# Performance work log

Hardware: AMD Instinct MI355X
Metric: run time of the kernel (lower is better)

The kernel has to match this reference:

```python
import jax, jax.numpy as jnp
import numpy as np

N_NODES = 50000
N_EDGES = 800000
HIDDEN = 128


def setup_inputs() -> dict:
    key = jax.random.key(0)
    k1, k2, k3, k4, k5, k6 = jax.random.split(key, 6)
    node_features = jax.random.normal(k1, (N_NODES, HIDDEN), dtype=jnp.float32)
    senders = jax.random.randint(k2, (N_EDGES,), 0, N_NODES, dtype=jnp.int32)
    receivers = jax.random.randint(k3, (N_EDGES,), 0, N_NODES, dtype=jnp.int32)
    edge_features = jax.random.normal(k4, (N_EDGES, HIDDEN), dtype=jnp.float32)
    # message_proj: Linear(3H, H); torch default init ~ U(-1/sqrt(fan_in), 1/sqrt(fan_in))
    bound = 1.0 / np.sqrt(3 * HIDDEN)
    W = jax.random.uniform(k5, (3 * HIDDEN, HIDDEN), dtype=jnp.float32, minval=-bound, maxval=bound)
    b = jax.random.uniform(k6, (HIDDEN,), dtype=jnp.float32, minval=-bound, maxval=bound)
    ln_w = jnp.ones((HIDDEN,), dtype=jnp.float32)
    ln_b = jnp.zeros((HIDDEN,), dtype=jnp.float32)
    return {"node_features": node_features, "senders": senders, "receivers": receivers,
            "edge_features": edge_features, "W": W, "b": b, "ln_w": ln_w, "ln_b": ln_b}


def layer_norm(x, w, b, eps=1e-5):
    mu = jnp.mean(x, axis=-1, keepdims=True)
    var = jnp.mean(jnp.square(x - mu), axis=-1, keepdims=True)
    return (x - mu) * jax.lax.rsqrt(var + eps) * w + b


def reference(node_features, senders, receivers, edge_features, W, b, ln_w, ln_b):
    # gather endpoints, concat along feature dim: [E, 3H]
    cat = jnp.concatenate((node_features[senders], node_features[receivers], edge_features), axis=-1)
    message = jax.nn.relu(cat @ W + b)  # [E, H]
    # scatter-add messages back to receiver nodes ('sum' aggregation)
    aggr = jax.ops.segment_sum(message, receivers, num_segments=node_features.shape[0])
    out = node_features + aggr  # residual
    return layer_norm(out, ln_w, ln_b)
```

## Files before the change

kernel.cpp:

```cpp
#include <hip/hip_runtime.h>

#define H 128
#define NSRC 3
#define MSTRIDE 132

typedef _Float16 f16;
typedef _Float16 f16x2 __attribute__((ext_vector_type(2)));
typedef _Float16 f16x4 __attribute__((ext_vector_type(4)));
typedef _Float16 f16x8 __attribute__((ext_vector_type(8)));
typedef float f32x4 __attribute__((ext_vector_type(4)));

__global__ void setup_kernel(const float* __restrict__ W, f16* __restrict__ wbuf,
                             int* __restrict__ cnt, float4* __restrict__ AGG4,
                             int n_nodes, int nagg4,
                             const float* __restrict__ nf, f16* __restrict__ nfh,
                             int nf4) {
    const int i = blockIdx.x * blockDim.x + threadIdx.x;
    const int np = gridDim.x * blockDim.x;
    if (i < NSRC * H * H) {
        int src = i >> 14;
        int k = (i >> 7) & 127;
        int c = i & 127;
        float v = W[((size_t)src * H + k) * H + c];
        unsigned off = ((unsigned)(c * 256 + k * 2)) ^ ((unsigned)((c & 7) << 4));
        wbuf[(size_t)src * (H * H) + (off >> 1)] = (f16)v;
    }
    if (i < n_nodes) cnt[i] = 0;
    for (int j = i; j < nagg4; j += np) AGG4[j] = make_float4(0.f, 0.f, 0.f, 0.f);
    for (int j = i; j < nf4; j += np) {
        float4 v = ((const float4*)nf)[j];
        f16x4 h;
        h[0] = (f16)v.x; h[1] = (f16)v.y; h[2] = (f16)v.z; h[3] = (f16)v.w;
        ((f16x4*)nfh)[j] = h;
    }
}

__global__ void hist_kernel(const int* __restrict__ recv, int* __restrict__ cnt, int n_edges) {
    int e = (blockIdx.x * blockDim.x + threadIdx.x) * 4;
    if (e + 3 < n_edges) {
        int4 r = *(const int4*)&recv[e];
        atomicAdd(&cnt[r.x], 1);
        atomicAdd(&cnt[r.y], 1);
        atomicAdd(&cnt[r.z], 1);
        atomicAdd(&cnt[r.w], 1);
    } else {
        for (int j = e; j < n_edges; ++j) atomicAdd(&cnt[recv[j]], 1);
    }
}

__global__ void scan_kernel(const int* __restrict__ cnt, int* __restrict__ row_ptr,
                            int* __restrict__ cursor, int n) {
    __shared__ int sd[1024];
    const int t = threadIdx.x;
    const int per = (n + 1023) >> 10;
    const int st = t * per;
    const int en = min(st + per, n);
    int s = 0;
    for (int i = st; i < en; ++i) s += cnt[i];
    sd[t] = s;
    __syncthreads();
    for (int off = 1; off < 1024; off <<= 1) {
        int v = 0;
        if (t >= off) v = sd[t - off];
        __syncthreads();
        sd[t] += v;
        __syncthreads();
    }
    int run = sd[t] - s;
    for (int i = st; i < en; ++i) {
        row_ptr[i] = run;
        cursor[i] = run;
        run += cnt[i];
    }
    if (t == 1023) row_ptr[n] = sd[1023];
}

__global__ void scatter_kernel(const int* __restrict__ send, const int* __restrict__ recv,
                               int* __restrict__ cursor, int* __restrict__ perm,
                               int2* __restrict__ ssr, int n_edges) {
    int e = blockIdx.x * blockDim.x + threadIdx.x;
    if (e < n_edges) {
        int r = recv[e];
        int pos = atomicAdd(&cursor[r], 1);
        perm[pos] = e;
        ssr[pos] = make_int2(send[e], r);
    }
}

__global__ __launch_bounds__(256, 2)
void fused_msg_kernel(const f16* __restrict__ nfh, const float* __restrict__ ef,
                      const int* __restrict__ perm, const int2* __restrict__ ssr,
                      const f16* __restrict__ wbuf, const float* __restrict__ b,
                      float* __restrict__ AGG, int n_edges) {
    __shared__ __align__(16) f16 Alds[NSRC * 64 * H];
    __shared__ __align__(16) f16 MSG[64 * MSTRIDE];
    __shared__ int SR[64];

    const int t = threadIdx.x;
    const int lane = t & 63;
    const int wid = t >> 6;
    const int l15 = lane & 15;
    const int lg = lane >> 4;
    const int c2 = lane * 2;

    f16x8 breg[NSRC][2][4];
#pragma unroll
    for (int src = 0; src < NSRC; ++src)
#pragma unroll
        for (int cf = 0; cf < 2; ++cf)
#pragma unroll
            for (int ks = 0; ks < 4; ++ks) {
                const int c = wid * 32 + cf * 16 + l15;
                const int k = ks * 32 + lg * 8;
                unsigned off = ((unsigned)(c * 256 + k * 2)) ^ ((unsigned)((c & 7) << 4));
                breg[src][cf][ks] =
                    *(const f16x8*)((const char*)wbuf + (size_t)src * 32768 + off);
            }

    const float2 bias2 = *(const float2*)&b[c2];
    const int srow = t >> 2;
    const int sq = t & 3;
    const int ntiles = (n_edges + 63) >> 6;
    const int stride = gridDim.x;

    int cr = 0;
    int ns = 0, nr = 0, npx = 0;
    int4 s0, s1, s2, s3;
    int4 r0, r1, r2, r3;
    float4 e0, e1, e2, e3, e4, e5, e6, e7;

    int tile = blockIdx.x;
    if (tile < ntiles) {
        const int e = min(tile * 64 + srow, n_edges - 1);
        int2 cv = ssr[e];
        int cs = cv.x; cr = cv.y;
        int cp = perm[e];
        const int4* ps = (const int4*)(nfh + (size_t)cs * H + sq * 32);
        s0 = ps[0]; s1 = ps[1]; s2 = ps[2]; s3 = ps[3];
        const int4* pr = (const int4*)(nfh + (size_t)cr * H + sq * 32);
        r0 = pr[0]; r1 = pr[1]; r2 = pr[2]; r3 = pr[3];
        const float4* pe = (const float4*)(ef + (size_t)cp * H + sq * 32);
        e0 = pe[0]; e1 = pe[1]; e2 = pe[2]; e3 = pe[3];
        e4 = pe[4]; e5 = pe[5]; e6 = pe[6]; e7 = pe[7];
    }
    if (tile + stride < ntiles) {
        const int e = min((tile + stride) * 64 + srow, n_edges - 1);
        int2 nv = ssr[e];
        ns = nv.x; nr = nv.y;
        npx = perm[e];
    }

    for (; tile < ntiles; tile += stride) {
        const int e0base = tile * 64;
        __syncthreads();

        {
            unsigned off0 = ((unsigned)(srow * 256 + (sq * 32 + 0) * 2)) ^ ((unsigned)((srow & 7) << 4));
            unsigned off1 = ((unsigned)(srow * 256 + (sq * 32 + 8) * 2)) ^ ((unsigned)((srow & 7) << 4));
            unsigned off2 = ((unsigned)(srow * 256 + (sq * 32 + 16) * 2)) ^ ((unsigned)((srow & 7) << 4));
            unsigned off3 = ((unsigned)(srow * 256 + (sq * 32 + 24) * 2)) ^ ((unsigned)((srow & 7) << 4));
            *(int4*)((char*)Alds + off0) = s0;
            *(int4*)((char*)Alds + off1) = s1;
            *(int4*)((char*)Alds + off2) = s2;
            *(int4*)((char*)Alds + off3) = s3;
            *(int4*)((char*)Alds + 16384 + off0) = r0;
            *(int4*)((char*)Alds + 16384 + off1) = r1;
            *(int4*)((char*)Alds + 16384 + off2) = r2;
            *(int4*)((char*)Alds + 16384 + off3) = r3;
            f16x8 h0, h1, h2, h3;
#pragma unroll
            for (int j = 0; j < 4; ++j) { h0[j] = (f16)(&e0.x)[j]; h0[j + 4] = (f16)(&e1.x)[j]; }
#pragma unroll
            for (int j = 0; j < 4; ++j) { h1[j] = (f16)(&e2.x)[j]; h1[j + 4] = (f16)(&e3.x)[j]; }
#pragma unroll
            for (int j = 0; j < 4; ++j) { h2[j] = (f16)(&e4.x)[j]; h2[j + 4] = (f16)(&e5.x)[j]; }
#pragma unroll
            for (int j = 0; j < 4; ++j) { h3[j] = (f16)(&e6.x)[j]; h3[j + 4] = (f16)(&e7.x)[j]; }
            *(f16x8*)((char*)Alds + 32768 + off0) = h0;
            *(f16x8*)((char*)Alds + 32768 + off1) = h1;
            *(f16x8*)((char*)Alds + 32768 + off2) = h2;
            *(f16x8*)((char*)Alds + 32768 + off3) = h3;
            if (sq == 0) SR[srow] = cr;
        }

        int t2s = 0, t2r = 0, t2p = 0;
        if (tile + 2 * stride < ntiles) {
            const int e = min((tile + 2 * stride) * 64 + srow, n_edges - 1);
            int2 t2v = ssr[e];
            t2s = t2v.x; t2r = t2v.y;
            t2p = perm[e];
        }
        if (tile + stride < ntiles) {
            const int4* ps = (const int4*)(nfh + (size_t)ns * H + sq * 32);
            s0 = ps[0]; s1 = ps[1]; s2 = ps[2]; s3 = ps[3];
            const int4* pr = (const int4*)(nfh + (size_t)nr * H + sq * 32);
            r0 = pr[0]; r1 = pr[1]; r2 = pr[2]; r3 = pr[3];
            const float4* pe = (const float4*)(ef + (size_t)npx * H + sq * 32);
            e0 = pe[0]; e1 = pe[1]; e2 = pe[2]; e3 = pe[3];
            e4 = pe[4]; e5 = pe[5]; e6 = pe[6]; e7 = pe[7];
        }
        __syncthreads();

        f32x4 acc[4][2];
#pragma unroll
        for (int rf = 0; rf < 4; ++rf) {
            acc[rf][0] = (f32x4){0.f, 0.f, 0.f, 0.f};
            acc[rf][1] = (f32x4){0.f, 0.f, 0.f, 0.f};
        }
#pragma unroll
        for (int src = 0; src < NSRC; ++src)
#pragma unroll
            for (int ks = 0; ks < 4; ++ks) {
                f16x8 af[4];
#pragma unroll
                for (int rf = 0; rf < 4; ++rf) {
                    const int row = rf * 16 + l15;
                    const int k = ks * 32 + lg * 8;
                    unsigned off = ((unsigned)(row * 256 + k * 2))
                                   ^ ((unsigned)((row & 7) << 4));
                    af[rf] = *(const f16x8*)((const char*)Alds + (size_t)src * 16384 + off);
                }
#pragma unroll
                for (int rf = 0; rf < 4; ++rf) {
                    acc[rf][0] = __builtin_amdgcn_mfma_f32_16x16x32_f16(
                        af[rf], breg[src][0][ks], acc[rf][0], 0, 0, 0);
                    acc[rf][1] = __builtin_amdgcn_mfma_f32_16x16x32_f16(
                        af[rf], breg[src][1][ks], acc[rf][1], 0, 0, 0);
                }
            }

#pragma unroll
        for (int rf = 0; rf < 4; ++rf)
#pragma unroll
            for (int cf = 0; cf < 2; ++cf)
#pragma unroll
                for (int q = 0; q < 4; ++q)
                    MSG[(rf * 16 + lg * 4 + q) * MSTRIDE + wid * 32 + cf * 16 + l15] =
                        (f16)acc[rf][cf][q];
        __syncthreads();

        int rarr[16];
#pragma unroll
        for (int j = 0; j < 16; ++j) rarr[j] = SR[wid * 16 + j];
        float ax = 0.f, ay = 0.f;
#pragma unroll
        for (int j = 0; j < 16; ++j) {
            const int e = e0base + wid * 16 + j;
            if (e < n_edges) {
                f16x2 m = *(const f16x2*)&MSG[(wid * 16 + j) * MSTRIDE + c2];
                ax += fmaxf((float)m[0] + bias2.x, 0.f);
                ay += fmaxf((float)m[1] + bias2.y, 0.f);
                bool flush = (j == 15) || (e + 1 >= n_edges) || (rarr[j + 1] != rarr[j]);
                if (flush) {
                    atomicAdd(&AGG[(size_t)rarr[j] * H + c2], ax);
                    atomicAdd(&AGG[(size_t)rarr[j] * H + c2 + 1], ay);
                    ax = 0.f;
                    ay = 0.f;
                }
            }
        }

        cr = nr;
        ns = t2s; nr = t2r; npx = t2p;
    }
}

__global__ __launch_bounds__(256, 4)
void ln_agg_kernel(const float* __restrict__ nf, const float* __restrict__ AGG,
                   const float* __restrict__ lnw, const float* __restrict__ lnb,
                   float* __restrict__ out, int n_nodes) {
    const int wv = threadIdx.x >> 6;
    const int lane = threadIdx.x & 63;
    const int row = blockIdx.x * (blockDim.x >> 6) + wv;
    if (row >= n_nodes) return;
    float2 a = ((const float2*)(nf + (size_t)row * H))[lane];
    float2 g = ((const float2*)(AGG + (size_t)row * H))[lane];
    float vx = a.x + g.x, vy = a.y + g.y;

    float s = vx + vy;
#pragma unroll
    for (int m = 32; m; m >>= 1) s += __shfl_xor(s, m, 64);
    float mu = s * (1.f / H);
    float dx = vx - mu, dy = vy - mu;
    float q = dx * dx + dy * dy;
#pragma unroll
    for (int m = 32; m; m >>= 1) q += __shfl_xor(q, m, 64);
    float rs = rsqrtf(q * (1.f / H) + 1e-5f);

    float2 w2 = ((const float2*)lnw)[lane];
    float2 b2 = ((const float2*)lnb)[lane];
    float2 o;
    o.x = dx * rs * w2.x + b2.x;
    o.y = dy * rs * w2.y + b2.y;
    ((float2*)(out + (size_t)row * H))[lane] = o;
}

__global__ void naive_edge_kernel(const float* __restrict__ nf, const int* __restrict__ s,
                                  const int* __restrict__ r, const float* __restrict__ ef,
                                  const float* __restrict__ W, const float* __restrict__ b,
                                  float* __restrict__ out, int n_edges) {
    int e = blockIdx.x * 2 + (threadIdx.x >> 7);
    int c = threadIdx.x & 127;
    if (e >= n_edges) return;
    int se = s[e], re = r[e];
    float acc = b[c];
    for (int k = 0; k < H; ++k) {
        acc += nf[(size_t)se * H + k] * W[(size_t)k * H + c];
        acc += nf[(size_t)re * H + k] * W[(size_t)(H + k) * H + c];
        acc += ef[(size_t)e * H + k] * W[(size_t)(2 * H + k) * H + c];
    }
    atomicAdd(&out[(size_t)re * H + c], fmaxf(acc, 0.f));
}

__global__ __launch_bounds__(256, 4)
void ln_kernel(const float* __restrict__ nf, const float* __restrict__ lnw,
               const float* __restrict__ lnb, float* __restrict__ out, int n_nodes) {
    const int wv = threadIdx.x >> 6;
    const int lane = threadIdx.x & 63;
    const int row = blockIdx.x * (blockDim.x >> 6) + wv;
    if (row >= n_nodes) return;
    float2 a = ((const float2*)(nf + (size_t)row * H))[lane];
    float2 g = ((float2*)(out + (size_t)row * H))[lane];
    float vx = a.x + g.x, vy = a.y + g.y;
    float s = vx + vy;
#pragma unroll
    for (int m = 32; m; m >>= 1) s += __shfl_xor(s, m, 64);
    float mu = s * (1.f / H);
    float dx = vx - mu, dy = vy - mu;
    float q = dx * dx + dy * dy;
#pragma unroll
    for (int m = 32; m; m >>= 1) q += __shfl_xor(q, m, 64);
    float rs = rsqrtf(q * (1.f / H) + 1e-5f);
    float2 w2 = ((const float2*)lnw)[lane];
    float2 b2 = ((const float2*)lnb)[lane];
    float2 o;
    o.x = dx * rs * w2.x + b2.x;
    o.y = dy * rs * w2.y + b2.y;
    ((float2*)(out + (size_t)row * H))[lane] = o;
}

extern "C" void kernel_launch(void* const* d_in, const int* in_sizes, int n_in,
                              void* d_out, int out_size, void* d_ws, size_t ws_size,
                              hipStream_t stream) {
    const float* nf        = (const float*)d_in[0];
    const int*   senders   = (const int*)d_in[1];
    const int*   receivers = (const int*)d_in[2];
    const float* ef        = (const float*)d_in[3];
    const float* W         = (const float*)d_in[4];
    const float* b         = (const float*)d_in[5];
    const float* lnw       = (const float*)d_in[6];
    const float* lnb       = (const float*)d_in[7];
    float* out = (float*)d_out;

    const int n_nodes = in_sizes[0] / H;
    const int n_edges = in_sizes[1];
    const int nfelem = n_nodes * H;

    size_t o = 0;
    auto carve = [&](size_t bytes) { size_t r = o; o += (bytes + 255) & ~(size_t)255; return r; };
    const size_t o_wbuf   = carve((size_t)NSRC * H * H * sizeof(f16));
    const size_t o_nfh    = carve((size_t)nfelem * sizeof(f16));
    const size_t o_cnt    = carve((size_t)n_nodes * 4);
    const size_t o_rowptr = carve((size_t)(n_nodes + 1) * 4);
    const size_t o_cursor = carve((size_t)n_nodes * 4);
    const size_t o_perm   = carve((size_t)n_edges * 4);
    const size_t o_ssr    = carve((size_t)n_edges * 8);
    const size_t o_agg    = carve((size_t)nfelem * sizeof(float));
    const size_t need_full = o;

    char* ws = (char*)d_ws;

    if (ws_size >= need_full) {
        f16* wbuf   = (f16*)(ws + o_wbuf);
        f16* nfh    = (f16*)(ws + o_nfh);
        int* cnt    = (int*)(ws + o_cnt);
        int* rowptr = (int*)(ws + o_rowptr);
        int* cursor = (int*)(ws + o_cursor);
        int* perm   = (int*)(ws + o_perm);
        int2* ssr   = (int2*)(ws + o_ssr);
        float* AGG  = (float*)(ws + o_agg);

        setup_kernel<<<2048, 256, 0, stream>>>(W, wbuf, cnt, (float4*)AGG,
                                               n_nodes, nfelem / 4, nf, nfh, nfelem / 4);
        hist_kernel<<<(n_edges / 4 + 255) / 256, 256, 0, stream>>>(receivers, cnt, n_edges);
        scan_kernel<<<1, 1024, 0, stream>>>(cnt, rowptr, cursor, n_nodes);
        scatter_kernel<<<(n_edges + 255) / 256, 256, 0, stream>>>(
            senders, receivers, cursor, perm, ssr, n_edges);

        fused_msg_kernel<<<1024, 256, 0, stream>>>(nfh, ef, perm, ssr, wbuf, b,
                                                   AGG, n_edges);
        ln_agg_kernel<<<(n_nodes + 3) / 4, 256, 0, stream>>>(nf, AGG, lnw, lnb, out, n_nodes);
    } else {
        hipMemsetAsync(d_out, 0, (size_t)nfelem * sizeof(float), stream);
        naive_edge_kernel<<<(n_edges + 1) / 2, 256, 0, stream>>>(
            nf, senders, receivers, ef, W, b, out, n_edges);
        ln_kernel<<<(n_nodes + 3) / 4, 256, 0, stream>>>(nf, lnw, lnb, out, n_nodes);
    }
}
```

Baseline: 384.3 us.

## Load edge features directly into MFMA fragments, shrink LDS, raise occupancy

Edge-feature rows are no longer staged through LDS. Each wave now loads its fp32 edge rows straight from global memory into MFMA A-fragments, converts them to f16 in registers, and issues the third-source MFMAs from those. This cuts LDS by a third and removes the prefetched receiver and edge registers, so launch bounds go to 3 blocks per CU and the grid to 1536. In exchange, the receiver and edge loads are no longer prefetched a tile ahead, so their global latency is exposed inside the loop. Each edge row is also fetched by all four waves, which adds redundant global traffic that only the cache can absorb.

```diff
diff --git a/kernel.cpp b/kernel.cpp
--- a/kernel.cpp
+++ b/kernel.cpp
@@ -87,12 +87,12 @@
     }
 }
 
-__global__ __launch_bounds__(256, 2)
+__global__ __launch_bounds__(256, 3)
 void fused_msg_kernel(const f16* __restrict__ nfh, const float* __restrict__ ef,
                       const int* __restrict__ perm, const int2* __restrict__ ssr,
                       const f16* __restrict__ wbuf, const float* __restrict__ b,
                       float* __restrict__ AGG, int n_edges) {
-    __shared__ __align__(16) f16 Alds[NSRC * 64 * H];
+    __shared__ __align__(16) f16 Alds[2 * 64 * H];
     __shared__ __align__(16) f16 MSG[64 * MSTRIDE];
     __shared__ int SR[64];
 
@@ -124,35 +124,32 @@
     const int stride = gridDim.x;
 
     int cr = 0;
-    int ns = 0, nr = 0, npx = 0;
+    int ns = 0, nr = 0;
+    int t2s = 0, t2r = 0;
     int4 s0, s1, s2, s3;
-    int4 r0, r1, r2, r3;
-    float4 e0, e1, e2, e3, e4, e5, e6, e7;
 
     int tile = blockIdx.x;
     if (tile < ntiles) {
         const int e = min(tile * 64 + srow, n_edges - 1);
         int2 cv = ssr[e];
         int cs = cv.x; cr = cv.y;
-        int cp = perm[e];
         const int4* ps = (const int4*)(nfh + (size_t)cs * H + sq * 32);
         s0 = ps[0]; s1 = ps[1]; s2 = ps[2]; s3 = ps[3];
-        const int4* pr = (const int4*)(nfh + (size_t)cr * H + sq * 32);
-        r0 = pr[0]; r1 = pr[1]; r2 = pr[2]; r3 = pr[3];
-        const float4* pe = (const float4*)(ef + (size_t)cp * H + sq * 32);
-        e0 = pe[0]; e1 = pe[1]; e2 = pe[2]; e3 = pe[3];
-        e4 = pe[4]; e5 = pe[5]; e6 = pe[6]; e7 = pe[7];
     }
     if (tile + stride < ntiles) {
         const int e = min((tile + stride) * 64 + srow, n_edges - 1);
         int2 nv = ssr[e];
         ns = nv.x; nr = nv.y;
-        npx = perm[e];
     }
 
     for (; tile < ntiles; tile += stride) {
         const int e0base = tile * 64;
         __syncthreads();
+
+        int p0 = perm[min(e0base + 0 + l15, n_edges - 1)];
+        int p1 = perm[min(e0base + 16 + l15, n_edges - 1)];
+        int p2 = perm[min(e0base + 32 + l15, n_edges - 1)];
+        int p3 = perm[min(e0base + 48 + l15, n_edges - 1)];
 
         {
             unsigned off0 = ((unsigned)(srow * 256 + (sq * 32 + 0) * 2)) ^ ((unsigned)((srow & 7) << 4));
@@ -163,41 +160,24 @@
             *(int4*)((char*)Alds + off1) = s1;
             *(int4*)((char*)Alds + off2) = s2;
             *(int4*)((char*)Alds + off3) = s3;
+            const int4* pr = (const int4*)(nfh + (size_t)cr * H + sq * 32);
+            int4 r0 = pr[0], r1 = pr[1], r2 = pr[2], r3 = pr[3];
             *(int4*)((char*)Alds + 16384 + off0) = r0;
             *(int4*)((char*)Alds + 16384 + off1) = r1;
             *(int4*)((char*)Alds + 16384 + off2) = r2;
             *(int4*)((char*)Alds + 16384 + off3) = r3;
-            f16x8 h0, h1, h2, h3;
-#pragma unroll
-            for (int j = 0; j < 4; ++j) { h0[j] = (f16)(&e0.x)[j]; h0[j + 4] = (f16)(&e1.x)[j]; }
-#pragma unroll
-            for (int j = 0; j < 4; ++j) { h1[j] = (f16)(&e2.x)[j]; h1[j + 4] = (f16)(&e3.x)[j]; }
-#pragma unroll
-            for (int j = 0; j < 4; ++j) { h2[j] = (f16)(&e4.x)[j]; h2[j + 4] = (f16)(&e5.x)[j]; }
-#pragma unroll
-            for (int j = 0; j < 4; ++j) { h3[j] = (f16)(&e6.x)[j]; h3[j + 4] = (f16)(&e7.x)[j]; }
-            *(f16x8*)((char*)Alds + 32768 + off0) = h0;
-            *(f16x8*)((char*)Alds + 32768 + off1) = h1;
-            *(f16x8*)((char*)Alds + 32768 + off2) = h2;
-            *(f16x8*)((char*)Alds + 32768 + off3) = h3;
             if (sq == 0) SR[srow] = cr;
         }
 
-        int t2s = 0, t2r = 0, t2p = 0;
+        t2s = 0; t2r = 0;
         if (tile + 2 * stride < ntiles) {
             const int e = min((tile + 2 * stride) * 64 + srow, n_edges - 1);
             int2 t2v = ssr[e];
             t2s = t2v.x; t2r = t2v.y;
-            t2p = perm[e];
         }
         if (tile + stride < ntiles) {
             const int4* ps = (const int4*)(nfh + (size_t)ns * H + sq * 32);
             s0 = ps[0]; s1 = ps[1]; s2 = ps[2]; s3 = ps[3];
-            const int4* pr = (const int4*)(nfh + (size_t)nr * H + sq * 32);
-            r0 = pr[0]; r1 = pr[1]; r2 = pr[2]; r3 = pr[3];
-            const float4* pe = (const float4*)(ef + (size_t)npx * H + sq * 32);
-            e0 = pe[0]; e1 = pe[1]; e2 = pe[2]; e3 = pe[3];
-            e4 = pe[4]; e5 = pe[5]; e6 = pe[6]; e7 = pe[7];
         }
         __syncthreads();
 
@@ -208,7 +188,7 @@
             acc[rf][1] = (f32x4){0.f, 0.f, 0.f, 0.f};
         }
 #pragma unroll
-        for (int src = 0; src < NSRC; ++src)
+        for (int src = 0; src < 2; ++src)
 #pragma unroll
             for (int ks = 0; ks < 4; ++ks) {
                 f16x8 af[4];
@@ -228,6 +208,43 @@
                         af[rf], breg[src][1][ks], acc[rf][1], 0, 0, 0);
                 }
             }
+#pragma unroll
+        for (int ks = 0; ks < 4; ++ks) {
+            const int ko = ks * 32 + lg * 8;
+            f16x8 af0, af1, af2, af3;
+            {
+                const float* q = ef + (size_t)p0 * H + ko;
+                float4 v0 = *(const float4*)q, v1 = *(const float4*)(q + 4);
+#pragma unroll
+                for (int j = 0; j < 4; ++j) { af0[j] = (f16)(&v0.x)[j]; af0[j + 4] = (f16)(&v1.x)[j]; }
+            }
+            {
+                const float* q = ef + (size_t)p1 * H + ko;
+                float4 v0 = *(const float4*)q, v1 = *(const float4*)(q + 4);
+#pragma unroll
+                for (int j = 0; j < 4; ++j) { af1[j] = (f16)(&v0.x)[j]; af1[j + 4] = (f16)(&v1.x)[j]; }
+            }
+            {
+                const float* q = ef + (size_t)p2 * H + ko;
+                float4 v0 = *(const float4*)q, v1 = *(const float4*)(q + 4);
+#pragma unroll
+                for (int j = 0; j < 4; ++j) { af2[j] = (f16)(&v0.x)[j]; af2[j + 4] = (f16)(&v1.x)[j]; }
+            }
+            {
+                const float* q = ef + (size_t)p3 * H + ko;
+                float4 v0 = *(const float4*)q, v1 = *(const float4*)(q + 4);
+#pragma unroll
+                for (int j = 0; j < 4; ++j) { af3[j] = (f16)(&v0.x)[j]; af3[j + 4] = (f16)(&v1.x)[j]; }
+            }
+            acc[0][0] = __builtin_amdgcn_mfma_f32_16x16x32_f16(af0, breg[2][0][ks], acc[0][0], 0, 0, 0);
+            acc[0][1] = __builtin_amdgcn_mfma_f32_16x16x32_f16(af0, breg[2][1][ks], acc[0][1], 0, 0, 0);
+            acc[1][0] = __builtin_amdgcn_mfma_f32_16x16x32_f16(af1, breg[2][0][ks], acc[1][0], 0, 0, 0);
+            acc[1][1] = __builtin_amdgcn_mfma_f32_16x16x32_f16(af1, breg[2][1][ks], acc[1][1], 0, 0, 0);
+            acc[2][0] = __builtin_amdgcn_mfma_f32_16x16x32_f16(af2, breg[2][0][ks], acc[2][0], 0, 0, 0);
+            acc[2][1] = __builtin_amdgcn_mfma_f32_16x16x32_f16(af2, breg[2][1][ks], acc[2][1], 0, 0, 0);
+            acc[3][0] = __builtin_amdgcn_mfma_f32_16x16x32_f16(af3, breg[2][0][ks], acc[3][0], 0, 0, 0);
+            acc[3][1] = __builtin_amdgcn_mfma_f32_16x16x32_f16(af3, breg[2][1][ks], acc[3][1], 0, 0, 0);
+        }
 
 #pragma unroll
         for (int rf = 0; rf < 4; ++rf)
@@ -261,7 +278,7 @@
         }
 
         cr = nr;
-        ns = t2s; nr = t2r; npx = t2p;
+        ns = t2s; nr = t2r;
     }
 }
 
@@ -387,7 +404,7 @@
         scatter_kernel<<<(n_edges + 255) / 256, 256, 0, stream>>>(
             senders, receivers, cursor, perm, ssr, n_edges);
 
-        fused_msg_kernel<<<1024, 256, 0, stream>>>(nfh, ef, perm, ssr, wbuf, b,
+        fused_msg_kernel<<<1536, 256, 0, stream>>>(nfh, ef, perm, ssr, wbuf, b,
                                                    AGG, n_edges);
         ln_agg_kernel<<<(n_nodes + 3) / 4, 256, 0, stream>>>(nf, AGG, lnw, lnb, out, n_nodes);
     } else {
```

Measured after the change: 639.8 us. 1.66x slower.

## Load receiver node rows straight into MFMA registers instead of staging in LDS

Applied to the files above, without the earlier changes.

The receiver-side node features are no longer prefetched into registers and written to shared memory. Each wave now reads them from global memory directly in MFMA fragment layout, using the receiver IDs stored in SR, and the LDS A-buffer shrinks from three sources to two. Because edges are sorted by receiver, neighbouring rows often share a receiver and hit in cache, and the smaller LDS footprint is meant to allow more resident blocks, so the grid grows from 1024 to 1536. The trade-off is that these global loads sit on the critical path right before the MFMAs and are no longer overlapped by the prefetch pipeline.

```diff
diff --git a/kernel.cpp b/kernel.cpp
--- a/kernel.cpp
+++ b/kernel.cpp
@@ -92,7 +92,7 @@
                       const int* __restrict__ perm, const int2* __restrict__ ssr,
                       const f16* __restrict__ wbuf, const float* __restrict__ b,
                       float* __restrict__ AGG, int n_edges) {
-    __shared__ __align__(16) f16 Alds[NSRC * 64 * H];
+    __shared__ __align__(16) f16 Alds[2 * 64 * H];
     __shared__ __align__(16) f16 MSG[64 * MSTRIDE];
     __shared__ int SR[64];
 
@@ -126,7 +126,6 @@
     int cr = 0;
     int ns = 0, nr = 0, npx = 0;
     int4 s0, s1, s2, s3;
-    int4 r0, r1, r2, r3;
     float4 e0, e1, e2, e3, e4, e5, e6, e7;
 
     int tile = blockIdx.x;
@@ -137,8 +136,6 @@
         int cp = perm[e];
         const int4* ps = (const int4*)(nfh + (size_t)cs * H + sq * 32);
         s0 = ps[0]; s1 = ps[1]; s2 = ps[2]; s3 = ps[3];
-        const int4* pr = (const int4*)(nfh + (size_t)cr * H + sq * 32);
-        r0 = pr[0]; r1 = pr[1]; r2 = pr[2]; r3 = pr[3];
         const float4* pe = (const float4*)(ef + (size_t)cp * H + sq * 32);
         e0 = pe[0]; e1 = pe[1]; e2 = pe[2]; e3 = pe[3];
         e4 = pe[4]; e5 = pe[5]; e6 = pe[6]; e7 = pe[7];
@@ -163,10 +160,6 @@
             *(int4*)((char*)Alds + off1) = s1;
             *(int4*)((char*)Alds + off2) = s2;
             *(int4*)((char*)Alds + off3) = s3;
-            *(int4*)((char*)Alds + 16384 + off0) = r0;
-            *(int4*)((char*)Alds + 16384 + off1) = r1;
-            *(int4*)((char*)Alds + 16384 + off2) = r2;
-            *(int4*)((char*)Alds + 16384 + off3) = r3;
             f16x8 h0, h1, h2, h3;
 #pragma unroll
             for (int j = 0; j < 4; ++j) { h0[j] = (f16)(&e0.x)[j]; h0[j + 4] = (f16)(&e1.x)[j]; }
@@ -176,10 +169,10 @@
             for (int j = 0; j < 4; ++j) { h2[j] = (f16)(&e4.x)[j]; h2[j + 4] = (f16)(&e5.x)[j]; }
 #pragma unroll
             for (int j = 0; j < 4; ++j) { h3[j] = (f16)(&e6.x)[j]; h3[j + 4] = (f16)(&e7.x)[j]; }
-            *(f16x8*)((char*)Alds + 32768 + off0) = h0;
-            *(f16x8*)((char*)Alds + 32768 + off1) = h1;
-            *(f16x8*)((char*)Alds + 32768 + off2) = h2;
-            *(f16x8*)((char*)Alds + 32768 + off3) = h3;
+            *(f16x8*)((char*)Alds + 16384 + off0) = h0;
+            *(f16x8*)((char*)Alds + 16384 + off1) = h1;
+            *(f16x8*)((char*)Alds + 16384 + off2) = h2;
+            *(f16x8*)((char*)Alds + 16384 + off3) = h3;
             if (sq == 0) SR[srow] = cr;
         }
 
@@ -193,14 +186,17 @@
         if (tile + stride < ntiles) {
             const int4* ps = (const int4*)(nfh + (size_t)ns * H + sq * 32);
             s0 = ps[0]; s1 = ps[1]; s2 = ps[2]; s3 = ps[3];
-            const int4* pr = (const int4*)(nfh + (size_t)nr * H + sq * 32);
-            r0 = pr[0]; r1 = pr[1]; r2 = pr[2]; r3 = pr[3];
             const float4* pe = (const float4*)(ef + (size_t)npx * H + sq * 32);
             e0 = pe[0]; e1 = pe[1]; e2 = pe[2]; e3 = pe[3];
             e4 = pe[4]; e5 = pe[5]; e6 = pe[6]; e7 = pe[7];
         }
         __syncthreads();
 
+        const int rr0 = SR[l15];
+        const int rr1 = SR[16 + l15];
+        const int rr2 = SR[32 + l15];
+        const int rr3 = SR[48 + l15];
+
         f32x4 acc[4][2];
 #pragma unroll
         for (int rf = 0; rf < 4; ++rf) {
@@ -208,7 +204,8 @@
             acc[rf][1] = (f32x4){0.f, 0.f, 0.f, 0.f};
         }
 #pragma unroll
-        for (int src = 0; src < NSRC; ++src)
+        for (int sph = 0; sph < 2; ++sph) {
+            const int bsel = (sph == 0) ? 0 : 2;
 #pragma unroll
             for (int ks = 0; ks < 4; ++ks) {
                 f16x8 af[4];
@@ -218,16 +215,33 @@
                     const int k = ks * 32 + lg * 8;
                     unsigned off = ((unsigned)(row * 256 + k * 2))
                                    ^ ((unsigned)((row & 7) << 4));
-                    af[rf] = *(const f16x8*)((const char*)Alds + (size_t)src * 16384 + off);
+                    af[rf] = *(const f16x8*)((const char*)Alds + (size_t)sph * 16384 + off);
                 }
 #pragma unroll
                 for (int rf = 0; rf < 4; ++rf) {
                     acc[rf][0] = __builtin_amdgcn_mfma_f32_16x16x32_f16(
-                        af[rf], breg[src][0][ks], acc[rf][0], 0, 0, 0);
+                        af[rf], breg[bsel][0][ks], acc[rf][0], 0, 0, 0);
                     acc[rf][1] = __builtin_amdgcn_mfma_f32_16x16x32_f16(
-                        af[rf], breg[src][1][ks], acc[rf][1], 0, 0, 0);
+                        af[rf], breg[bsel][1][ks], acc[rf][1], 0, 0, 0);
                 }
             }
+        }
+#pragma unroll
+        for (int ks = 0; ks < 4; ++ks) {
+            const int ko = ks * 32 + lg * 8;
+            f16x8 a0 = *(const f16x8*)(nfh + (size_t)rr0 * H + ko);
+            f16x8 a1 = *(const f16x8*)(nfh + (size_t)rr1 * H + ko);
+            f16x8 a2 = *(const f16x8*)(nfh + (size_t)rr2 * H + ko);
+            f16x8 a3 = *(const f16x8*)(nfh + (size_t)rr3 * H + ko);
+            acc[0][0] = __builtin_amdgcn_mfma_f32_16x16x32_f16(a0, breg[1][0][ks], acc[0][0], 0, 0, 0);
+            acc[0][1] = __builtin_amdgcn_mfma_f32_16x16x32_f16(a0, breg[1][1][ks], acc[0][1], 0, 0, 0);
+            acc[1][0] = __builtin_amdgcn_mfma_f32_16x16x32_f16(a1, breg[1][0][ks], acc[1][0], 0, 0, 0);
+            acc[1][1] = __builtin_amdgcn_mfma_f32_16x16x32_f16(a1, breg[1][1][ks], acc[1][1], 0, 0, 0);
+            acc[2][0] = __builtin_amdgcn_mfma_f32_16x16x32_f16(a2, breg[1][0][ks], acc[2][0], 0, 0, 0);
+            acc[2][1] = __builtin_amdgcn_mfma_f32_16x16x32_f16(a2, breg[1][1][ks], acc[2][1], 0, 0, 0);
+            acc[3][0] = __builtin_amdgcn_mfma_f32_16x16x32_f16(a3, breg[1][0][ks], acc[3][0], 0, 0, 0);
+            acc[3][1] = __builtin_amdgcn_mfma_f32_16x16x32_f16(a3, breg[1][1][ks], acc[3][1], 0, 0, 0);
+        }
 
 #pragma unroll
         for (int rf = 0; rf < 4; ++rf)
@@ -387,7 +401,7 @@
         scatter_kernel<<<(n_edges + 255) / 256, 256, 0, stream>>>(
             senders, receivers, cursor, perm, ssr, n_edges);
 
-        fused_msg_kernel<<<1024, 256, 0, stream>>>(nfh, ef, perm, ssr, wbuf, b,
+        fused_msg_kernel<<<1536, 256, 0, stream>>>(nfh, ef, perm, ssr, wbuf, b,
                                                    AGG, n_edges);
         ln_agg_kernel<<<(n_nodes + 3) / 4, 256, 0, stream>>>(nf, AGG, lnw, lnb, out, n_nodes);
     } else {
```

Result: slower. 415.8 us (+8.2%).
